# Performance work log

Measured on AMD Instinct MI355X. Metric: run time of the kernel, lower is better.

The kernel has to match this reference:

```python
import jax, jax.numpy as jnp
import numpy as np

DIM = 512
W = 64            # windowSize
R = 128           # receptiveSize
H = 8             # numHeads
HD = 64           # headDim
MAXD = W - 1 + (R - W) // 2  # maxDisparity = 95


def setup_inputs() -> dict:
    key = jax.random.key(0)
    ks = jax.random.split(key, 12)
    B_ = 512
    inp = {
        'x':  jax.random.normal(ks[0], (B_, 1 + W, DIM), jnp.float32),
        'x_': jax.random.normal(ks[1], (B_, 1 + R, DIM), jnp.float32),
        'mask_left':  jax.random.randint(ks[2], (4, 1 + W, 1 + R), 0, 2, jnp.int32),
        'mask_right': jax.random.randint(ks[3], (4, 1 + W, 1 + R), 0, 2, jnp.int32),
        'nW': 64,
        'rel_table': jax.random.normal(ks[4], (2 * MAXD + 1, H), jnp.float32) * 0.02,
        'cls_self':  jax.random.normal(ks[5], (1, H, 1, 1), jnp.float32) * 0.02,
        'cls_up':    jax.random.normal(ks[6], (1, H, 1, R), jnp.float32) * 0.02,
        'cls_down':  jax.random.normal(ks[7], (1, H, W, 1), jnp.float32) * 0.02,
        'Wq':  jax.random.normal(ks[8], (H * HD, DIM), jnp.float32) * 0.02,
        'bq':  jnp.zeros((H * HD,), jnp.float32),
        'Wkv': jax.random.normal(ks[9], (2 * H * HD, DIM), jnp.float32) * 0.02,
        'bkv': jnp.zeros((2 * H * HD,), jnp.float32),
        'Wp':  jax.random.normal(ks[10], (DIM, H * HD), jnp.float32) * 0.02,
        'bp':  jnp.zeros((DIM,), jnp.float32),
    }
    return inp


def _attention(x, x_, mask_left, mask_right, nW, rel_table, cls_self, cls_up,
               cls_down, Wq, bq, Wkv, bkv, Wp, bp):
    B_, n, C = x.shape   # n = 1+W
    m = x_.shape[1]      # m = 1+R
    B = B_ // nW
    scale = HD ** -0.5

    q = x @ Wq.T + bq                                  # (B_, n, H*HD)
    kv = x_ @ Wkv.T + bkv                              # (B_, m, 2*H*HD)
    k, v = jnp.split(kv, 2, axis=-1)
    q = q.reshape(B_, n, H, HD).transpose(0, 2, 1, 3)  # (B_, H, n, d)
    k = k.reshape(B_, m, H, HD).transpose(0, 2, 1, 3)
    v = v.reshape(B_, m, H, HD).transpose(0, 2, 1, 3)

    attn = jnp.einsum('bhnd,bhmd->bhnm', q, k) * scale  # (B_, H, n, m)

    # relative position bias gathered from the table
    coords = jnp.arange(W)[:, None] - (jnp.arange(R) - (R - W) // 2)[None, :] + MAXD
    rel_bias = rel_table[coords]                       # (W, R, H)
    rel_bias = rel_bias.transpose(2, 0, 1)             # (H, W, R)

    # assemble full (H, n, m) bias: cls-self | cls-up row ; cls-down col | rel body
    top = jnp.concatenate([cls_self[0], cls_up[0]], axis=2)       # (H, 1, 1+R)
    bot = jnp.concatenate([cls_down[0], rel_bias], axis=2)        # (H, W, 1+R)
    bias = jnp.concatenate([top, bot], axis=1)                    # (H, n, m)
    attn = attn + bias[None]

    # boundary-window masking
    mask_value = -jnp.finfo(attn.dtype).max
    attn = attn.reshape(B, nW, H, n, m)
    mc = min(mask_left.shape[0], nW)
    ml = mask_left[:mc][None, :, None]    # (1, mc, 1, n, m)
    mr = mask_right[-mc:][None, :, None]
    attn = attn.at[:, :mc].set(jnp.where(ml == 1, mask_value, attn[:, :mc]))
    attn = attn.at[:, nW - mc:].set(jnp.where(mr == 1, mask_value, attn[:, nW - mc:]))
    attn = attn.reshape(B_, H, n, m)

    attn = jax.nn.softmax(attn, axis=-1)
    out = jnp.einsum('bhnm,bhmd->bhnd', attn, v)       # (B_, H, n, d)
    out = out.transpose(0, 2, 1, 3).reshape(B_, n, H * HD)
    return out @ Wp.T + bp                             # (B_, n, C)


def reference(x, x_, mask_left, mask_right, nW, rel_table, cls_self, cls_up,
              cls_down, Wq, bq, Wkv, bkv, Wp, bp):
    return _attention(x, x_, mask_left, mask_right, nW, rel_table, cls_self,
                      cls_up, cls_down, Wq, bq, Wkv, bkv, Wp, bp)
```

## Files before the change

### kernel.cpp

```cpp
#include <hip/hip_runtime.h>
#include <float.h>

#define DIMC 512
#define WW 64
#define RR 128
#define NH 8
#define HDIM 64
#define NSEQ 65
#define MSEQ 129

typedef __attribute__((ext_vector_type(8))) short short8;
typedef __attribute__((ext_vector_type(4))) float f32x4;
typedef __attribute__((ext_vector_type(4))) unsigned int u32x4;
typedef __attribute__((ext_vector_type(4))) unsigned short u16x4;

typedef __attribute__((address_space(3))) unsigned int lds_uint;
typedef __attribute__((address_space(1))) unsigned int glob_uint;

__device__ __forceinline__ float asfloat(unsigned int u) { union { unsigned int i; float f; } v; v.i = u; return v.f; }
__device__ __forceinline__ unsigned int asuint(float f) { union { float f; unsigned int i; } v; v.f = f; return v.i; }
__device__ __forceinline__ unsigned short f2bf(float f) {
  unsigned int x = asuint(f);
  x += 0x7fffu + ((x >> 16) & 1u);
  return (unsigned short)(x >> 16);
}
__device__ __forceinline__ float bf2f(unsigned short b) { return asfloat(((unsigned int)b) << 16); }

__device__ __forceinline__ short8 ld_b64x2(const unsigned short* p) {
  typedef __attribute__((ext_vector_type(4))) short sh4;
  sh4 lo = *(const sh4*)p;
  sh4 hi = *(const sh4*)(p + 4);
  short8 r;
  r[0] = lo[0]; r[1] = lo[1]; r[2] = lo[2]; r[3] = lo[3];
  r[4] = hi[0]; r[5] = hi[1]; r[6] = hi[2]; r[7] = hi[3];
  return r;
}

__global__ void convert_f32_bf16(const float* __restrict__ s,
                                 unsigned short* __restrict__ d, long n4) {
  long stride = (long)gridDim.x * blockDim.x;
  for (long i = (long)blockIdx.x * blockDim.x + threadIdx.x; i < n4; i += stride) {
    f32x4 f = ((const f32x4*)s)[i];
    u16x4 o;
    o[0] = f2bf(f[0]); o[1] = f2bf(f[1]); o[2] = f2bf(f[2]); o[3] = f2bf(f[3]);
    ((u16x4*)d)[i] = o;
  }
}

template<int OUTBF>
__global__ __launch_bounds__(256)
void gemm_nt(const unsigned short* __restrict__ A, const unsigned short* __restrict__ Bw,
             const float* __restrict__ bias, void* __restrict__ Cout,
             long M, long N, long K) {
  __shared__ unsigned short As[128 * 64];
  __shared__ unsigned short Bs[128 * 64];
  const int tid  = threadIdx.x;
  const int lane = tid & 63;
  const int wid  = tid >> 6;
  const int wr   = wid >> 1, wc = wid & 1;
  const long mBase = (long)blockIdx.y * 128;
  const long nBase = (long)blockIdx.x * 128;
  const int r15 = lane & 15;
  const int g16 = lane >> 4;

  f32x4 acc[4][4];
#pragma unroll
  for (int a = 0; a < 4; ++a)
#pragma unroll
    for (int b = 0; b < 4; ++b) acc[a][b] = (f32x4){0.f, 0.f, 0.f, 0.f};

  const int srow = tid >> 3;
  const int skb  = (tid & 7) * 8;

  for (long kt = 0; kt < K; kt += 64) {
    __syncthreads();
#pragma unroll
    for (int j = 0; j < 4; ++j) {
      long row = j * 32 + srow;
      const unsigned short* ga = A  + (mBase + row) * K + kt + skb;
      const unsigned short* gb = Bw + (nBase + row) * K + kt + skb;
      __builtin_amdgcn_global_load_lds((glob_uint*)ga, (lds_uint*)(As + (j * 256 + wid * 64) * 8), 16, 0, 0);
      __builtin_amdgcn_global_load_lds((glob_uint*)gb, (lds_uint*)(Bs + (j * 256 + wid * 64) * 8), 16, 0, 0);
    }
    __syncthreads();
#pragma unroll
    for (int kk = 0; kk < 64; kk += 32) {
      short8 af[4], bfr[4];
#pragma unroll
      for (int mi = 0; mi < 4; ++mi)
        af[mi] = *(const short8*)&As[(wr * 64 + mi * 16 + r15) * 64 + kk + g16 * 8];
#pragma unroll
      for (int ni = 0; ni < 4; ++ni)
        bfr[ni] = *(const short8*)&Bs[(wc * 64 + ni * 16 + r15) * 64 + kk + g16 * 8];
#pragma unroll
      for (int mi = 0; mi < 4; ++mi)
#pragma unroll
        for (int ni = 0; ni < 4; ++ni)
          acc[mi][ni] = __builtin_amdgcn_mfma_f32_16x16x32_bf16(af[mi], bfr[ni], acc[mi][ni], 0, 0, 0);
    }
  }

  float bv[4];
  long col[4];
#pragma unroll
  for (int ni = 0; ni < 4; ++ni) { col[ni] = nBase + wc * 64 + ni * 16 + r15; bv[ni] = bias[col[ni]]; }
#pragma unroll
  for (int mi = 0; mi < 4; ++mi) {
    long row0 = mBase + wr * 64 + mi * 16 + g16 * 4;
#pragma unroll
    for (int ni = 0; ni < 4; ++ni) {
#pragma unroll
      for (int v = 0; v < 4; ++v) {
        float val = acc[mi][ni][v] + bv[ni];
        long off = (row0 + v) * N + col[ni];
        if (OUTBF) ((unsigned short*)Cout)[off] = f2bf(val);
        else       ((float*)Cout)[off] = val;
      }
    }
  }
}

#define VT_OFF 0
#define VT_STR 140
#define K_OFF  (64 * VT_STR)
#define Q_OFF  (K_OFF + 144 * 64)
#define P_OFF  K_OFF
#define P_STR  136
#define SMEM_ELEMS (Q_OFF + 80 * 64)

__global__ __launch_bounds__(256, 3)
void attn_mfma(const unsigned short* __restrict__ qb,
               const unsigned short* __restrict__ kvb,
               unsigned short* __restrict__ aob,
               const float* __restrict__ rel_table,
               const float* __restrict__ cls_self,
               const float* __restrict__ cls_up,
               const float* __restrict__ cls_down,
               const int* __restrict__ mask_left,
               const int* __restrict__ mask_right,
               const int* __restrict__ nWp, int mcL) {
  __shared__ unsigned short smem[SMEM_ELEMS];
  const int h   = blockIdx.x;
  const int b_  = blockIdx.y;
  const int tid = threadIdx.x, lane = tid & 63, wid = tid >> 6;
  const int r15 = lane & 15, g16 = lane >> 4;

  const int nW = nWp[0];
  const int w  = b_ % nW;
  const int mc = min(mcL, nW);
  const bool useL = (w < mc);
  const bool useR = (w >= nW - mc);
  const int wR = mcL - mc + (w - (nW - mc));

  const unsigned short* kgbase = kvb + (long)b_ * MSEQ * (2 * DIMC) + h * HDIM;
  const unsigned short* vgbase = kgbase + DIMC;
  const unsigned short* qgbase = qb  + (long)b_ * NSEQ * DIMC + h * HDIM;

  const int lr  = lane >> 3;
  const int lcs = ((lane & 7) ^ (lr & 7)) * 8;
#pragma unroll
  for (int j = 0; j < 4; ++j) {
    int chunk = j * 4 + wid;
    int gr = chunk * 8 + lr;
    __builtin_amdgcn_global_load_lds((glob_uint*)(kgbase + (long)gr * (2 * DIMC) + lcs),
                                     (lds_uint*)(smem + K_OFF + chunk * 512), 16, 0, 0);
  }
  if (wid == 0) {
    __builtin_amdgcn_global_load_lds((glob_uint*)(kgbase + (long)128 * (2 * DIMC) + lcs),
                                     (lds_uint*)(smem + K_OFF + 16 * 512), 16, 0, 0);
  }
#pragma unroll
  for (int j = 0; j < 2; ++j) {
    int chunk = j * 4 + wid;
    int gr = chunk * 8 + lr;
    __builtin_amdgcn_global_load_lds((glob_uint*)(qgbase + (long)gr * DIMC + lcs),
                                     (lds_uint*)(smem + Q_OFF + chunk * 512), 16, 0, 0);
  }
  if (wid < 2) {
    int chunk = 8 + wid;
    int gr = min(chunk * 8 + lr, NSEQ - 1);
    __builtin_amdgcn_global_load_lds((glob_uint*)(qgbase + (long)gr * DIMC + lcs),
                                     (lds_uint*)(smem + Q_OFF + chunk * 512), 16, 0, 0);
  }
  for (int it = 0; it < 5; ++it) {
    int idx = it * 256 + tid;
    if (idx < MSEQ * 8) {
      int c = idx >> 3, d0 = (idx & 7) * 8;
      u32x4 u = *(const u32x4*)(vgbase + (long)c * (2 * DIMC) + d0);
#pragma unroll
      for (int jj = 0; jj < 4; ++jj) {
        smem[VT_OFF + (d0 + 2 * jj) * VT_STR + c]     = (unsigned short)(u[jj] & 0xffffu);
        smem[VT_OFF + (d0 + 2 * jj + 1) * VT_STR + c] = (unsigned short)(u[jj] >> 16);
      }
    }
  }
  __syncthreads();

  f32x4 S[2][9];
  const int swz = (r15 & 7) << 3;
#pragma unroll
  for (int t = 0; t < 2; ++t) {
    if (t == 1 && wid != 0) continue;
    const int i0 = (t == 0 ? wid : 4) * 16;
    short8 a0 = *(const short8*)&smem[Q_OFF + (i0 + r15) * 64 + ((g16 * 8) ^ swz)];
    short8 a1 = *(const short8*)&smem[Q_OFF + (i0 + r15) * 64 + ((32 + g16 * 8) ^ swz)];
#pragma unroll
    for (int ni = 0; ni < 9; ++ni) {
      short8 b0 = *(const short8*)&smem[K_OFF + (ni * 16 + r15) * 64 + ((g16 * 8) ^ swz)];
      short8 b1 = *(const short8*)&smem[K_OFF + (ni * 16 + r15) * 64 + ((32 + g16 * 8) ^ swz)];
      f32x4 c = (f32x4){0.f, 0.f, 0.f, 0.f};
      c = __builtin_amdgcn_mfma_f32_16x16x32_bf16(a0, b0, c, 0, 0, 0);
      c = __builtin_amdgcn_mfma_f32_16x16x32_bf16(a1, b1, c, 0, 0, 0);
      S[t][ni] = c;
    }
  }
  __syncthreads();

  float p128[2][4];
#pragma unroll
  for (int t = 0; t < 2; ++t) {
    if (t == 1 && wid != 0) continue;
    const int i0 = (t == 0 ? wid : 4) * 16;
#pragma unroll
    for (int v = 0; v < 4; ++v) {
      int row  = i0 + g16 * 4 + v;
      int rowb = min(row, NSEQ - 1);
#pragma unroll
      for (int ni = 0; ni < 9; ++ni) {
        int col = ni * 16 + r15;
        float val;
        if (col > 128) {
          val = -FLT_MAX;
        } else {
          float bias;
          if (row == 0) bias = (col == 0) ? cls_self[h] : cls_up[h * RR + col - 1];
          else bias = (col == 0) ? cls_down[h * WW + rowb - 1]
                                 : rel_table[min(rowb - col + 127, 190) * NH + h];
          val = S[t][ni][v] * 0.125f + bias;
          if (useL && mask_left[((long)w * NSEQ + rowb) * MSEQ + col])  val = -FLT_MAX;
          if (useR && mask_right[((long)wR * NSEQ + rowb) * MSEQ + col]) val = -FLT_MAX;
        }
        S[t][ni][v] = val;
      }
    }
#pragma unroll
    for (int v = 0; v < 4; ++v) {
      float m = S[t][0][v];
#pragma unroll
      for (int ni = 1; ni < 9; ++ni) m = fmaxf(m, S[t][ni][v]);
#pragma unroll
      for (int off = 1; off < 16; off <<= 1) m = fmaxf(m, __shfl_xor(m, off, 64));
      float sum = 0.f;
#pragma unroll
      for (int ni = 0; ni < 9; ++ni) {
        float p = __expf(S[t][ni][v] - m);
        S[t][ni][v] = p;
        sum += p;
      }
#pragma unroll
      for (int off = 1; off < 16; off <<= 1) sum += __shfl_xor(sum, off, 64);
      float inv = 1.0f / sum;
#pragma unroll
      for (int ni = 0; ni < 9; ++ni) S[t][ni][v] *= inv;
    }
#pragma unroll
    for (int ni = 0; ni < 8; ++ni)
#pragma unroll
      for (int v = 0; v < 4; ++v)
        smem[P_OFF + (i0 + g16 * 4 + v) * P_STR + ni * 16 + r15] = f2bf(S[t][ni][v]);
#pragma unroll
    for (int v = 0; v < 4; ++v) p128[t][v] = S[t][8][v];
  }
  __syncthreads();

#pragma unroll
  for (int t = 0; t < 2; ++t) {
    if (t == 1 && wid != 0) continue;
    const int i0 = (t == 0 ? wid : 4) * 16;
    short8 pa[4];
#pragma unroll
    for (int kk = 0; kk < 4; ++kk)
      pa[kk] = *(const short8*)&smem[P_OFF + (i0 + r15) * P_STR + kk * 32 + g16 * 8];
    f32x4 acc[4];
#pragma unroll
    for (int nt = 0; nt < 4; ++nt) acc[nt] = (f32x4){0.f, 0.f, 0.f, 0.f};
#pragma unroll
    for (int nt = 0; nt < 4; ++nt)
#pragma unroll
      for (int kk = 0; kk < 4; ++kk) {
        short8 bv = ld_b64x2(&smem[VT_OFF + (nt * 16 + r15) * VT_STR + kk * 32 + g16 * 8]);
        acc[nt] = __builtin_amdgcn_mfma_f32_16x16x32_bf16(pa[kk], bv, acc[nt], 0, 0, 0);
      }
    float p1b[4];
#pragma unroll
    for (int v = 0; v < 4; ++v) p1b[v] = __shfl(p128[t][v], (lane & 48), 64);
#pragma unroll
    for (int nt = 0; nt < 4; ++nt) {
      float v128 = bf2f(smem[VT_OFF + (nt * 16 + r15) * VT_STR + 128]);
#pragma unroll
      for (int v = 0; v < 4; ++v) {
        int row = i0 + g16 * 4 + v;
        if (row < NSEQ) {
          float o = acc[nt][v] + p1b[v] * v128;
          aob[((long)b_ * NSEQ + row) * DIMC + h * HDIM + nt * 16 + r15] = f2bf(o);
        }
      }
    }
  }
}

extern "C" void kernel_launch(void* const* d_in, const int* in_sizes, int n_in,
                              void* d_out, int out_size, void* d_ws, size_t ws_size,
                              hipStream_t stream) {
  const float* x          = (const float*)d_in[0];
  const float* x_         = (const float*)d_in[1];
  const int*   mask_left  = (const int*)d_in[2];
  const int*   mask_right = (const int*)d_in[3];
  const int*   nWp        = (const int*)d_in[4];
  const float* rel_table  = (const float*)d_in[5];
  const float* cls_self   = (const float*)d_in[6];
  const float* cls_up     = (const float*)d_in[7];
  const float* cls_down   = (const float*)d_in[8];
  const float* Wq         = (const float*)d_in[9];
  const float* bq         = (const float*)d_in[10];
  const float* Wkv        = (const float*)d_in[11];
  const float* bkv        = (const float*)d_in[12];
  const float* Wp         = (const float*)d_in[13];
  const float* bp         = (const float*)d_in[14];

  const long B_  = in_sizes[0] / (NSEQ * DIMC);
  const int  mcL = in_sizes[2] / (NSEQ * MSEQ);
  const long Mq  = B_ * NSEQ;
  const long Mkv = B_ * MSEQ;

  unsigned short* xb    = (unsigned short*)d_ws;
  unsigned short* x_b   = xb    + Mq  * DIMC;
  unsigned short* wqb   = x_b   + Mkv * DIMC;
  unsigned short* wkvb  = wqb   + DIMC * DIMC;
  unsigned short* wpb   = wkvb  + 2 * DIMC * DIMC;
  unsigned short* qbuf  = wpb   + DIMC * DIMC;
  unsigned short* kvbuf = qbuf  + Mq  * DIMC;
  unsigned short* aob   = kvbuf + Mkv * 2 * DIMC;
  const size_t needed = (size_t)(Mq * DIMC * 3 + Mkv * DIMC * 3 + 4 * DIMC * DIMC) * 2;
  if (ws_size < needed) return;

  auto cv = [&](const float* s, unsigned short* d, long n) {
    long n4 = n / 4;
    int blocks = (int)((n4 + 255) / 256); if (blocks > 8192) blocks = 8192;
    convert_f32_bf16<<<blocks, 256, 0, stream>>>(s, d, n4);
  };
  cv(x,   xb,   Mq * DIMC);
  cv(x_,  x_b,  Mkv * DIMC);
  cv(Wq,  wqb,  (long)DIMC * DIMC);
  cv(Wkv, wkvb, 2L * DIMC * DIMC);
  cv(Wp,  wpb,  (long)DIMC * DIMC);

  gemm_nt<1><<<dim3(DIMC / 128, (unsigned)(Mq / 128)), 256, 0, stream>>>(
      xb, wqb, bq, qbuf, Mq, DIMC, DIMC);
  gemm_nt<1><<<dim3(2 * DIMC / 128, (unsigned)(Mkv / 128)), 256, 0, stream>>>(
      x_b, wkvb, bkv, kvbuf, Mkv, 2 * DIMC, DIMC);

  attn_mfma<<<dim3(NH, (unsigned)B_), 256, 0, stream>>>(
      qbuf, kvbuf, aob, rel_table, cls_self, cls_up, cls_down,
      mask_left, mask_right, nWp, mcL);

  gemm_nt<0><<<dim3(DIMC / 128, (unsigned)(Mq / 128)), 256, 0, stream>>>(
      aob, wpb, bp, d_out, Mq, DIMC, DIMC);
}
```

Baseline: 640.8 us.

## Shrink attention LDS footprint, load Q from global, remap GEMM tiles across XCDs

The attention kernel stops staging Q in LDS and reads the MFMA A-operands straight from global memory. It also holds V in registers and transposes it into LDS only after the QK^T MFMAs, reusing the freed region and raising the occupancy target from 3 to 4 blocks per CU. The P write-back is moved after an extra barrier so it does not overwrite K while other waves may still be reading it. The GEMMs switch to a 1D grid with an XCD-aware block remap, meant to improve L2 locality on the multi-die MI355X, at the cost of some extra register pressure and an added sync.

```diff
diff --git a/kernel.cpp b/kernel.cpp
--- a/kernel.cpp
+++ b/kernel.cpp
@@ -51,15 +51,21 @@
 __global__ __launch_bounds__(256)
 void gemm_nt(const unsigned short* __restrict__ A, const unsigned short* __restrict__ Bw,
              const float* __restrict__ bias, void* __restrict__ Cout,
-             long M, long N, long K) {
+             long M, long N, long K, int gx) {
   __shared__ unsigned short As[128 * 64];
   __shared__ unsigned short Bs[128 * 64];
+  const int nwg  = gridDim.x;
+  const int orig = blockIdx.x;
+  const int q8 = nwg >> 3, r8 = nwg & 7;
+  const int xcd = orig & 7, sub = orig >> 3;
+  const int wg = (xcd < r8 ? xcd * (q8 + 1) : r8 * (q8 + 1) + (xcd - r8) * q8) + sub;
+  const long nBase = (long)(wg % gx) * 128;
+  const long mBase = (long)(wg / gx) * 128;
+
   const int tid  = threadIdx.x;
   const int lane = tid & 63;
   const int wid  = tid >> 6;
   const int wr   = wid >> 1, wc = wid & 1;
-  const long mBase = (long)blockIdx.y * 128;
-  const long nBase = (long)blockIdx.x * 128;
   const int r15 = lane & 15;
   const int g16 = lane >> 4;
 
@@ -123,12 +129,11 @@
 #define VT_OFF 0
 #define VT_STR 140
 #define K_OFF  (64 * VT_STR)
-#define Q_OFF  (K_OFF + 144 * 64)
 #define P_OFF  K_OFF
 #define P_STR  136
-#define SMEM_ELEMS (Q_OFF + 80 * 64)
-
-__global__ __launch_bounds__(256, 3)
+#define SMEM_ELEMS (K_OFF + 80 * P_STR)
+
+__global__ __launch_bounds__(256, 4)
 void attn_mfma(const unsigned short* __restrict__ qb,
                const unsigned short* __restrict__ kvb,
                unsigned short* __restrict__ aob,
@@ -169,32 +174,17 @@
     __builtin_amdgcn_global_load_lds((glob_uint*)(kgbase + (long)128 * (2 * DIMC) + lcs),
                                      (lds_uint*)(smem + K_OFF + 16 * 512), 16, 0, 0);
   }
-#pragma unroll
-  for (int j = 0; j < 2; ++j) {
-    int chunk = j * 4 + wid;
-    int gr = chunk * 8 + lr;
-    __builtin_amdgcn_global_load_lds((glob_uint*)(qgbase + (long)gr * DIMC + lcs),
-                                     (lds_uint*)(smem + Q_OFF + chunk * 512), 16, 0, 0);
-  }
-  if (wid < 2) {
-    int chunk = 8 + wid;
-    int gr = min(chunk * 8 + lr, NSEQ - 1);
-    __builtin_amdgcn_global_load_lds((glob_uint*)(qgbase + (long)gr * DIMC + lcs),
-                                     (lds_uint*)(smem + Q_OFF + chunk * 512), 16, 0, 0);
-  }
+  __syncthreads();
+
+  u32x4 vreg[5];
+#pragma unroll
   for (int it = 0; it < 5; ++it) {
     int idx = it * 256 + tid;
     if (idx < MSEQ * 8) {
       int c = idx >> 3, d0 = (idx & 7) * 8;
-      u32x4 u = *(const u32x4*)(vgbase + (long)c * (2 * DIMC) + d0);
-#pragma unroll
-      for (int jj = 0; jj < 4; ++jj) {
-        smem[VT_OFF + (d0 + 2 * jj) * VT_STR + c]     = (unsigned short)(u[jj] & 0xffffu);
-        smem[VT_OFF + (d0 + 2 * jj + 1) * VT_STR + c] = (unsigned short)(u[jj] >> 16);
-      }
-    }
-  }
-  __syncthreads();
+      vreg[it] = *(const u32x4*)(vgbase + (long)c * (2 * DIMC) + d0);
+    }
+  }
 
   f32x4 S[2][9];
   const int swz = (r15 & 7) << 3;
@@ -202,8 +192,10 @@
   for (int t = 0; t < 2; ++t) {
     if (t == 1 && wid != 0) continue;
     const int i0 = (t == 0 ? wid : 4) * 16;
-    short8 a0 = *(const short8*)&smem[Q_OFF + (i0 + r15) * 64 + ((g16 * 8) ^ swz)];
-    short8 a1 = *(const short8*)&smem[Q_OFF + (i0 + r15) * 64 + ((32 + g16 * 8) ^ swz)];
+    const int qrow = min(i0 + r15, NSEQ - 1);
+    const unsigned short* qp = qgbase + (long)qrow * DIMC;
+    short8 a0 = *(const short8*)(qp + g16 * 8);
+    short8 a1 = *(const short8*)(qp + 32 + g16 * 8);
 #pragma unroll
     for (int ni = 0; ni < 9; ++ni) {
       short8 b0 = *(const short8*)&smem[K_OFF + (ni * 16 + r15) * 64 + ((g16 * 8) ^ swz)];
@@ -214,7 +206,20 @@
       S[t][ni] = c;
     }
   }
-  __syncthreads();
+
+#pragma unroll
+  for (int it = 0; it < 5; ++it) {
+    int idx = it * 256 + tid;
+    if (idx < MSEQ * 8) {
+      int c = idx >> 3, d0 = (idx & 7) * 8;
+      u32x4 u = vreg[it];
+#pragma unroll
+      for (int jj = 0; jj < 4; ++jj) {
+        smem[VT_OFF + (d0 + 2 * jj) * VT_STR + c]     = (unsigned short)(u[jj] & 0xffffu);
+        smem[VT_OFF + (d0 + 2 * jj + 1) * VT_STR + c] = (unsigned short)(u[jj] >> 16);
+      }
+    }
+  }
 
   float p128[2][4];
 #pragma unroll
@@ -264,12 +269,19 @@
       for (int ni = 0; ni < 9; ++ni) S[t][ni][v] *= inv;
     }
 #pragma unroll
+    for (int v = 0; v < 4; ++v) p128[t][v] = S[t][8][v];
+  }
+  __syncthreads();
+
+#pragma unroll
+  for (int t = 0; t < 2; ++t) {
+    if (t == 1 && wid != 0) continue;
+    const int i0 = (t == 0 ? wid : 4) * 16;
+#pragma unroll
     for (int ni = 0; ni < 8; ++ni)
 #pragma unroll
       for (int v = 0; v < 4; ++v)
         smem[P_OFF + (i0 + g16 * 4 + v) * P_STR + ni * 16 + r15] = f2bf(S[t][ni][v]);
-#pragma unroll
-    for (int v = 0; v < 4; ++v) p128[t][v] = S[t][8][v];
   }
   __syncthreads();
 
@@ -355,15 +367,21 @@
   cv(Wkv, wkvb, 2L * DIMC * DIMC);
   cv(Wp,  wpb,  (long)DIMC * DIMC);
 
-  gemm_nt<1><<<dim3(DIMC / 128, (unsigned)(Mq / 128)), 256, 0, stream>>>(
-      xb, wqb, bq, qbuf, Mq, DIMC, DIMC);
-  gemm_nt<1><<<dim3(2 * DIMC / 128, (unsigned)(Mkv / 128)), 256, 0, stream>>>(
-      x_b, wkvb, bkv, kvbuf, Mkv, 2 * DIMC, DIMC);
+  {
+    int gx = DIMC / 128, nwg = (int)(gx * (Mq / 128));
+    gemm_nt<1><<<nwg, 256, 0, stream>>>(xb, wqb, bq, qbuf, Mq, DIMC, DIMC, gx);
+  }
+  {
+    int gx = 2 * DIMC / 128, nwg = (int)(gx * (Mkv / 128));
+    gemm_nt<1><<<nwg, 256, 0, stream>>>(x_b, wkvb, bkv, kvbuf, Mkv, 2 * DIMC, DIMC, gx);
+  }
 
   attn_mfma<<<dim3(NH, (unsigned)B_), 256, 0, stream>>>(
       qbuf, kvbuf, aob, rel_table, cls_self, cls_up, cls_down,
       mask_left, mask_right, nWp, mcL);
 
-  gemm_nt<0><<<dim3(DIMC / 128, (unsigned)(Mq / 128)), 256, 0, stream>>>(
-      aob, wpb, bp, d_out, Mq, DIMC, DIMC);
-}
+  {
+    int gx = DIMC / 128, nwg = (int)(gx * (Mq / 128));
+    gemm_nt<0><<<nwg, 256, 0, stream>>>(aob, wpb, bp, d_out, Mq, DIMC, DIMC, gx);
+  }
+}
```

Result: slower. 721.2 us (+12.6%).
